# Kernel tuning notes

Measured on AMD Instinct MI355X. Metric: run time of the kernel, lower is better.

Reference implementation:

```python
import jax, jax.numpy as jnp
import numpy as np

EPS_NORM = 1e-12  # F.normalize eps
EPS_BN = 1e-5     # BatchNorm2d eps


def _neighbor_idx(h, w):
    # Replicates get_window_mask's clamped 3x3 neighbor indices (hw, 9).
    off = np.array([-1, 0, 1])
    x_off = np.tile(off, 3)        # [-1,0,1,-1,0,1,-1,0,1]
    y_off = np.repeat(off, 3)      # [-1,-1,-1,0,0,0,1,1,1]
    yy, xx = np.meshgrid(np.arange(h), np.arange(w), indexing='ij')
    x_nn = np.clip(xx.reshape(-1, 1) + x_off[None, :], 0, w - 1)
    y_nn = np.clip(yy.reshape(-1, 1) + y_off[None, :], 0, h - 1)
    return jnp.asarray(y_nn * w + x_nn, dtype=jnp.int32)  # (hw, 9)


def _find_nn(xf, yf, idx):
    # Faithful to find_nn: cosine sim between cur pixel and 3x3 window of y,
    # argmin over the (masked-in) window, gather the NORMALIZED y feature.
    # The dense (hw,hw) matmul + 9999 mask reduces exactly to these 9 candidates.
    b, c, h, w = xf.shape
    xn = xf.reshape(b, c, h * w).transpose(0, 2, 1)  # (b, hw, c)
    xn = xn / jnp.maximum(jnp.linalg.norm(xn, axis=-1, keepdims=True), EPS_NORM)
    yn = yf.reshape(b, c, h * w)
    yn = yn / jnp.maximum(jnp.linalg.norm(yn, axis=1, keepdims=True), EPS_NORM)
    ynt = yn.transpose(0, 2, 1)          # (b, hw, c)
    y_nb = ynt[:, idx, :]                # (b, hw, 9, c) gathered neighbors
    sims = jnp.einsum('bpc,bpkc->bpk', xn, y_nb)  # (b, hw, 9)
    k = jnp.argmin(sims, axis=-1)
    nnv = jnp.take_along_axis(y_nb, k[:, :, None, None], axis=2)[:, :, 0, :]
    return nnv.transpose(0, 2, 1).reshape(b, c, h, w)


def _forward(x, conv_w, bn_gamma, bn_beta):
    h, w = x.shape[-2:]
    prev_f, next_f, cur_f = x[:, 0], x[:, 1], x[:, 2]
    idx = _neighbor_idx(h, w)
    nn_prev = _find_nn(cur_f, prev_f, idx)
    nn_next = _find_nn(cur_f, next_f, idx)
    feat = jnp.concatenate([nn_prev, nn_next, cur_f], axis=1)  # (b, 3c, h, w)
    out = jnp.einsum('oc,bchw->bohw', conv_w, feat)            # 1x1 conv, no bias
    # BatchNorm2d in training mode: per-channel batch stats (biased var)
    mean = out.mean(axis=(0, 2, 3), keepdims=True)
    var = out.var(axis=(0, 2, 3), keepdims=True)
    out = (out - mean) * jax.lax.rsqrt(var + EPS_BN)
    out = out * bn_gamma[None, :, None, None] + bn_beta[None, :, None, None]
    out = jax.nn.relu(out)
    return jnp.stack([prev_f, next_f, out], axis=1)  # (b, 3, c, h, w)


def setup_inputs() -> dict:
    key = jax.random.key(0)
    k1, k2 = jax.random.split(key)
    b, c, h, w = 8, 256, 64, 64
    x = jax.random.normal(k1, (b, 3, c, h, w), dtype=jnp.float32)
    fan_in, fan_out = 3 * c, c
    bound = float(np.sqrt(6.0 / (fan_in + fan_out)))  # xavier_uniform
    conv_w = jax.random.uniform(k2, (c, 3 * c), dtype=jnp.float32, minval=-bound, maxval=bound)
    bn_gamma = jnp.ones((c,), dtype=jnp.float32)
    bn_beta = jnp.zeros((c,), dtype=jnp.float32)
    return {'x': x, 'conv_w': conv_w, 'bn_gamma': bn_gamma, 'bn_beta': bn_beta}


def reference(x, conv_w, bn_gamma, bn_beta):
    return _forward(x, conv_w, bn_gamma, bn_beta)
```

## Files before the change

kernel.cpp:

```cpp
#include <hip/hip_runtime.h>

constexpr int B  = 8;
constexpr int C  = 256;
constexpr int Hh = 64;
constexpr int Ww = 64;
constexpr int P  = Hh * Ww;
constexpr int CP = C * P;
constexpr int CT = 3 * C;
constexpr int J  = B * P;

constexpr int DOT_D_OFF = 0;
constexpr int SSQ_D_OFF = 294912;
constexpr int IV_F_OFF  = 655360;
constexpr int SEL_F_OFF = 663552;
constexpr int SIV_F_OFF = 671744;
constexpr int WB_F_OFF  = 679936;

typedef __attribute__((ext_vector_type(8))) short short8;
typedef __attribute__((ext_vector_type(4))) float f32x4;

__device__ inline unsigned short bf16_rne(float f) {
    unsigned u = __float_as_uint(f);
    return (unsigned short)((u + 0x7fffu + ((u >> 16) & 1u)) >> 16);
}
__device__ inline unsigned pack2(float a, float b) {
    return (unsigned)bf16_rne(a) | ((unsigned)bf16_rne(b) << 16);
}

__global__ __launch_bounds__(256) void k_wcvt(const float* __restrict__ Wg,
                                              unsigned short* __restrict__ Wb) {
    int i = blockIdx.x * 256 + threadIdx.x;
    Wb[i] = bf16_rne(Wg[i]);
}

__global__ __launch_bounds__(256) void k_dots(const float* __restrict__ x,
                                              float* __restrict__ out) {
    __shared__ float ys[2][2][6][64];
    __shared__ float cs[2][256];
    const int t     = threadIdx.x;
    const int b     = blockIdx.x >> 4;
    const int strip = blockIdx.x & 15;
    const int chunk = blockIdx.y;
    const int y0 = strip * 4;
    const int ry = t >> 6;
    const int xc = t & 63;
    const int xm = max(xc - 1, 0), xp = min(xc + 1, 63);
    const int c0 = chunk * 64;

    size_t gbase; int l0;
    if (t < 64) {
        gbase = (size_t)(b * 3 + 2) * CP + (size_t)c0 * P + strip * 256 + t * 4;
        l0 = t * 4;
    } else {
        int i   = t - 64;
        int sid = i >= 96;
        int r   = (i - sid * 96) >> 4;
        int x4  = i & 15;
        int yl  = min(max(y0 - 1 + r, 0), Hh - 1);
        gbase = (size_t)(b * 3 + sid) * CP + (size_t)c0 * P + yl * 64 + x4 * 4;
        l0 = (sid * 6 + r) * 64 + x4 * 4;
    }
    float* ysf = &ys[0][0][0][0];
    float* dst0 = (t < 64) ? &cs[0][l0] : &ysf[l0];
    float* dst1 = (t < 64) ? &cs[1][l0] : &ysf[768 + l0];

    double d[2][9] = {{0,0,0,0,0,0,0,0,0},{0,0,0,0,0,0,0,0,0}};
    double qs[2] = {0.0, 0.0};

    f32x4 r0 = *(const f32x4*)(x + gbase);
    f32x4 r1 = *(const f32x4*)(x + gbase + (size_t)P);

    #define COMPUTE(BUF)                                                     \
    {                                                                        \
        double cd = (double)cs[BUF][t];                                      \
        _Pragma("unroll")                                                    \
        for (int s = 0; s < 2; ++s) {                                        \
            const float* Y0 = &ys[BUF][s][ry][0];             \
            const float* Y1 = Y0 + 64;                        \
            const float* Y2 = Y1 + 64;                        \
            d[s][0] = fma(cd, (double)Y0[xm], d[s][0]);                      \
            d[s][1] = fma(cd, (double)Y0[xc], d[s][1]);                      \
            d[s][2] = fma(cd, (double)Y0[xp], d[s][2]);                      \
            d[s][3] = fma(cd, (double)Y1[xm], d[s][3]);                      \
            d[s][4] = fma(cd, (double)Y1[xc], d[s][4]);                      \
            d[s][5] = fma(cd, (double)Y1[xp], d[s][5]);                      \
            d[s][6] = fma(cd, (double)Y2[xm], d[s][6]);                      \
            d[s][7] = fma(cd, (double)Y2[xc], d[s][7]);                      \
            d[s][8] = fma(cd, (double)Y2[xp], d[s][8]);                      \
            double ov = (double)Y1[xc];                                      \
            qs[s] = fma(ov, ov, qs[s]);                                      \
        }                                                                    \
    }

    for (int n = 0; n < 64; n += 2) {
        *(f32x4*)dst0 = r0;
        __syncthreads();
        if (n + 2 < 64)
            r0 = *(const f32x4*)(x + gbase + (size_t)(n + 2) * P);
        COMPUTE(0)
        *(f32x4*)dst1 = r1;
        __syncthreads();
        if (n + 3 < 64)
            r1 = *(const f32x4*)(x + gbase + (size_t)(n + 3) * P);
        COMPUTE(1)
    }
    #undef COMPUTE

    const int p = strip * 256 + t;
    double* db = (double*)(out + (size_t)(b * 3) * CP);
    #pragma unroll
    for (int s = 0; s < 2; ++s) {
        #pragma unroll
        for (int k = 0; k < 9; ++k)
            db[DOT_D_OFF + (size_t)((chunk * 2 + s) * 9 + k) * 4096 + p] = d[s][k];
        db[SSQ_D_OFF + (size_t)(chunk * 2 + s) * 4096 + p] = qs[s];
    }
}

__global__ __launch_bounds__(256) void k_iv(float* __restrict__ out) {
    int gid  = blockIdx.x * 256 + threadIdx.x;
    int side = gid >> 15;
    int j    = gid & (J - 1);
    int b = j >> 12, p = j & (P - 1);
    const double* sb = (const double*)(out + (size_t)(b * 3) * CP) + SSQ_D_OFF;
    double ssum = ((sb[(0 * 2 + side) * 4096 + p]
                  + sb[(1 * 2 + side) * 4096 + p])
                  + sb[(2 * 2 + side) * 4096 + p])
                  + sb[(3 * 2 + side) * 4096 + p];
    float* ivb = out + (size_t)(b * 3) * CP + IV_F_OFF;
    ivb[side * 4096 + p] = 1.0f / fmaxf((float)sqrt(ssum), 1e-12f);
}

__global__ __launch_bounds__(256) void k_sel(float* __restrict__ out) {
    int gid  = blockIdx.x * 256 + threadIdx.x;
    int side = gid >> 15;
    int j    = gid & (J - 1);
    int b = j >> 12, p = j & (P - 1);
    int y = p >> 6, xc = p & 63;

    int nidx[9];
    #pragma unroll
    for (int k = 0; k < 9; ++k) {
        int dy = k / 3 - 1, dx = k % 3 - 1;
        int yy = min(max(y + dy, 0), Hh - 1);
        int xx = min(max(xc + dx, 0), Ww - 1);
        nidx[k] = yy * Ww + xx;
    }

    const double* db  = (const double*)(out + (size_t)(b * 3) * CP) + DOT_D_OFF;
    const float*  ivb = out + (size_t)(b * 3) * CP + IV_F_OFF;

    double best = 0.0; int bi = 0;
    #pragma unroll
    for (int k = 0; k < 9; ++k) {
        double sk = ((db[(size_t)((0 * 2 + side) * 9 + k) * 4096 + p]
                    + db[(size_t)((1 * 2 + side) * 9 + k) * 4096 + p])
                    + db[(size_t)((2 * 2 + side) * 9 + k) * 4096 + p])
                    + db[(size_t)((3 * 2 + side) * 9 + k) * 4096 + p];
        double s = sk * (double)ivb[side * 4096 + nidx[k]];
        if (k == 0 || s < best) { best = s; bi = k; }
    }
    int*   selb = (int*)(out + (size_t)(b * 3) * CP + SEL_F_OFF);
    float* sivb = out + (size_t)(b * 3) * CP + SIV_F_OFF;
    selb[side * 4096 + p] = nidx[bi];
    sivb[side * 4096 + p] = ivb[side * 4096 + nidx[bi]];
}

__global__ __launch_bounds__(512) void k_gemm(const float* __restrict__ x,
                                              const unsigned short* __restrict__ Wb,
                                              float* __restrict__ out) {
    __shared__ unsigned short As[2][4][256][8];
    __shared__ unsigned short Bs[2][4][128][8];
    __shared__ int   sel_s[2][128];
    __shared__ float siv_s[2][128];

    const int t  = threadIdx.x;
    const int j0 = blockIdx.x * 128;
    const int b  = j0 >> 12, p0 = j0 & (P - 1);

    if (t < 256) {
        int side = t >> 7, jj = t & 127;
        const int*   selb = (const int*)(out + (size_t)(b * 3) * CP + SEL_F_OFF);
        const float* sivb = out + (size_t)(b * 3) * CP + SIV_F_OFF;
        sel_s[side][jj] = selb[side * 4096 + p0 + jj];
        siv_s[side][jj] = sivb[side * 4096 + p0 + jj];
    }
    __syncthreads();

    const int lane = t & 63, w = t >> 6;
    const int q = lane >> 4, l16 = lane & 15;
    const int m0w = (w & 3) * 64;
    const int n0w = (w >> 2) * 64;

    const int jj = t & 127, kq = (t >> 7) & 3;
    const int ma = t & 255, kh = t >> 8;
    const int k0 = kq * 8;

    const float* pp = x + (size_t)(b * 3 + 0) * CP + sel_s[0][jj];
    const float* np = x + (size_t)(b * 3 + 1) * CP + sel_s[1][jj];
    const float* cp = x + (size_t)(b * 3 + 2) * CP + p0 + jj;
    const float  sp = siv_s[0][jj], sn = siv_s[1][jj];
    const unsigned short* wbase = Wb + (size_t)ma * CT + kh * 16;

    f32x4 acc[4][4];
    #pragma unroll
    for (int f = 0; f < 4; ++f)
        #pragma unroll
        for (int g = 0; g < 4; ++g)
            acc[f][g] = (f32x4){0.f, 0.f, 0.f, 0.f};

    short8 wa0, wa1;
    float fb[8];
    float scale;

    #define LOAD_STEP(KK)                                                    \
    {                                                                        \
        const unsigned short* wsrc = wbase + (KK);                           \
        wa0 = *(const short8*)wsrc;                                          \
        wa1 = *(const short8*)(wsrc + 8);                                    \
        const float* src;                                                    \
        if ((KK) < 256)      { src = pp + (size_t)((KK) + k0) * P;       scale = sp;   } \
        else if ((KK) < 512) { src = np + (size_t)((KK) - 256 + k0) * P; scale = sn;   } \
        else                 { src = cp + (size_t)((KK) - 512 + k0) * P; scale = 1.0f; } \
        _Pragma("unroll")                                                    \
        for (int u = 0; u < 8; ++u) fb[u] = src[(size_t)u * P];              \
    }

    #define WRITE_STEP(BUF)                                                  \
    {                                                                        \
        *(short8*)&As[BUF][kh * 2    ][ma][0] = wa0;                         \
        *(short8*)&As[BUF][kh * 2 + 1][ma][0] = wa1;                         \
        uint4 pk = make_uint4(pack2(fb[0] * scale, fb[1] * scale),           \
                              pack2(fb[2] * scale, fb[3] * scale),           \
                              pack2(fb[4] * scale, fb[5] * scale),           \
                              pack2(fb[6] * scale, fb[7] * scale));          \
        *(uint4*)&Bs[BUF][kq][jj][0] = pk;                                   \
    }

    LOAD_STEP(0)
    WRITE_STEP(0)
    __syncthreads();

    for (int i = 0; i < 24; ++i) {
        if (i + 1 < 24) LOAD_STEP((i + 1) * 32)
        const int cur = i & 1;
        short8 af[4], bfr[4];
        #pragma unroll
        for (int f = 0; f < 4; ++f)
            af[f] = *(const short8*)&As[cur][q][m0w + f * 16 + l16][0];
        #pragma unroll
        for (int g = 0; g < 4; ++g)
            bfr[g] = *(const short8*)&Bs[cur][q][n0w + g * 16 + l16][0];
        #pragma unroll
        for (int f = 0; f < 4; ++f)
            #pragma unroll
            for (int g = 0; g < 4; ++g)
                acc[f][g] = __builtin_amdgcn_mfma_f32_16x16x32_bf16(
                    af[f], bfr[g], acc[f][g], 0, 0, 0);
        if (i + 1 < 24) WRITE_STEP((i + 1) & 1)
        __syncthreads();
    }
    #undef LOAD_STEP
    #undef WRITE_STEP

    float* outb = out + (size_t)(b * 3 + 2) * CP;
    #pragma unroll
    for (int f = 0; f < 4; ++f)
        #pragma unroll
        for (int g = 0; g < 4; ++g)
            #pragma unroll
            for (int r = 0; r < 4; ++r) {
                int ch  = m0w + f * 16 + q * 4 + r;
                int col = p0 + n0w + g * 16 + l16;
                outb[(size_t)ch * P + col] = acc[f][g][r];
            }
}

__global__ __launch_bounds__(256) void k_bn(float* __restrict__ out,
                                            const float* __restrict__ gamma,
                                            const float* __restrict__ beta) {
    __shared__ double rs[256], rq[256];
    __shared__ float sc_s, sh_s;
    const int o = blockIdx.x, t = threadIdx.x;

    double s = 0.0, q = 0.0;
    for (int b = 0; b < B; ++b) {
        const float4* base =
            (const float4*)(out + (size_t)(b * 3 + 2) * CP + (size_t)o * P);
        #pragma unroll
        for (int i = 0; i < 4; ++i) {
            float4 v = base[i * 256 + t];
            s += (double)v.x + (double)v.y + (double)v.z + (double)v.w;
            q += (double)v.x * v.x + (double)v.y * v.y
               + (double)v.z * v.z + (double)v.w * v.w;
        }
    }
    rs[t] = s; rq[t] = q;
    __syncthreads();
    for (int off = 128; off > 0; off >>= 1) {
        if (t < off) { rs[t] += rs[t + off]; rq[t] += rq[t + off]; }
        __syncthreads();
    }
    if (t == 0) {
        double mean = rs[0] * (1.0 / (double)J);
        double var  = rq[0] * (1.0 / (double)J) - mean * mean;
        double inv  = 1.0 / sqrt(var + 1e-5);
        double sc   = (double)gamma[o] * inv;
        sc_s = (float)sc;
        sh_s = (float)((double)beta[o] - mean * sc);
    }
    __syncthreads();
    const float sc = sc_s, sh = sh_s;

    for (int b = 0; b < B; ++b) {
        float4* base =
            (float4*)(out + (size_t)(b * 3 + 2) * CP + (size_t)o * P);
        #pragma unroll
        for (int i = 0; i < 4; ++i) {
            float4 v = base[i * 256 + t];
            v.x = fmaxf(fmaf(v.x, sc, sh), 0.f);
            v.y = fmaxf(fmaf(v.y, sc, sh), 0.f);
            v.z = fmaxf(fmaf(v.z, sc, sh), 0.f);
            v.w = fmaxf(fmaf(v.w, sc, sh), 0.f);
            base[i * 256 + t] = v;
        }
    }
}

__global__ __launch_bounds__(256) void k_copy(const float4* __restrict__ x4,
                                              float4* __restrict__ o4) {
    int tid = blockIdx.x * blockDim.x + threadIdx.x;
    const int per_b = 2 * CP / 4;
    const int bstr  = 3 * CP / 4;
    if (tid < B * per_b) {
        int b = tid / per_b;
        int r = tid - b * per_b;
        o4[b * bstr + r] = x4[b * bstr + r];
    }
}

extern "C" void kernel_launch(void* const* d_in, const int* in_sizes, int n_in,
                              void* d_out, int out_size, void* d_ws, size_t ws_size,
                              hipStream_t stream) {
    const float* x     = (const float*)d_in[0];
    const float* wconv = (const float*)d_in[1];
    const float* gamma = (const float*)d_in[2];
    const float* beta  = (const float*)d_in[3];
    float* out = (float*)d_out;
    (void)d_ws; (void)ws_size;

    unsigned short* Wbuf = (unsigned short*)(out + WB_F_OFF);

    k_wcvt<<<CT * C / 256, 256, 0, stream>>>(wconv, Wbuf);

    k_dots<<<dim3(128, 4), 256, 0, stream>>>(x, out);

    k_iv<<<2 * J / 256, 256, 0, stream>>>(out);

    k_sel<<<2 * J / 256, 256, 0, stream>>>(out);

    k_gemm<<<J / 128, 512, 0, stream>>>(x, Wbuf, out);

    k_bn<<<C, 256, 0, stream>>>(out, gamma, beta);

    k_copy<<<(B * 2 * CP / 4 + 255) / 256, 256, 0, stream>>>(
        (const float4*)x, (float4*)out);
}
```

Before: 267.5 us.

## Fuse inverse-norm kernel into selection and deepen k_dots channel pipeline

Removes the separate k_iv launch by recomputing each neighbor's inverse norm inside k_sel from the partial sum-of-squares buffers. This saves one kernel launch and one intermediate buffer round-trip, but adds redundant loads and sqrt work per neighbor. Separately, k_dots now stages two channels per shared-memory buffer, with four channels of global loads in flight. This halves the number of barriers per channel at the cost of more shared memory and registers.

Measured after the change: 262.0 us. 2.0% less time.

```diff
diff --git a/kernel.cpp b/kernel.cpp
--- a/kernel.cpp
+++ b/kernel.cpp
@@ -11,7 +11,6 @@
 
 constexpr int DOT_D_OFF = 0;
 constexpr int SSQ_D_OFF = 294912;
-constexpr int IV_F_OFF  = 655360;
 constexpr int SEL_F_OFF = 663552;
 constexpr int SIV_F_OFF = 671744;
 constexpr int WB_F_OFF  = 679936;
@@ -35,8 +34,8 @@
 
 __global__ __launch_bounds__(256) void k_dots(const float* __restrict__ x,
                                               float* __restrict__ out) {
-    __shared__ float ys[2][2][6][64];
-    __shared__ float cs[2][256];
+    __shared__ float ys[2][2][2][6][64];
+    __shared__ float cs[2][2][256];
     const int t     = threadIdx.x;
     const int b     = blockIdx.x >> 4;
     const int strip = blockIdx.x & 15;
@@ -47,10 +46,15 @@
     const int xm = max(xc - 1, 0), xp = min(xc + 1, 63);
     const int c0 = chunk * 64;
 
-    size_t gbase; int l0;
+    size_t gbase;
+    float *d00, *d01, *d10, *d11;
+    float* ysf = &ys[0][0][0][0][0];
+    float* csf = &cs[0][0][0];
     if (t < 64) {
         gbase = (size_t)(b * 3 + 2) * CP + (size_t)c0 * P + strip * 256 + t * 4;
-        l0 = t * 4;
+        int l0 = t * 4;
+        d00 = csf + l0;        d01 = csf + 256 + l0;
+        d10 = csf + 512 + l0;  d11 = csf + 768 + l0;
     } else {
         int i   = t - 64;
         int sid = i >= 96;
@@ -58,24 +62,25 @@
         int x4  = i & 15;
         int yl  = min(max(y0 - 1 + r, 0), Hh - 1);
         gbase = (size_t)(b * 3 + sid) * CP + (size_t)c0 * P + yl * 64 + x4 * 4;
-        l0 = (sid * 6 + r) * 64 + x4 * 4;
-    }
-    float* ysf = &ys[0][0][0][0];
-    float* dst0 = (t < 64) ? &cs[0][l0] : &ysf[l0];
-    float* dst1 = (t < 64) ? &cs[1][l0] : &ysf[768 + l0];
+        int l0 = (sid * 6 + r) * 64 + x4 * 4;
+        d00 = ysf + l0;         d01 = ysf + 768 + l0;
+        d10 = ysf + 1536 + l0;  d11 = ysf + 1536 + 768 + l0;
+    }
 
     double d[2][9] = {{0,0,0,0,0,0,0,0,0},{0,0,0,0,0,0,0,0,0}};
     double qs[2] = {0.0, 0.0};
 
-    f32x4 r0 = *(const f32x4*)(x + gbase);
-    f32x4 r1 = *(const f32x4*)(x + gbase + (size_t)P);
-
-    #define COMPUTE(BUF)                                                     \
+    f32x4 a0 = *(const f32x4*)(x + gbase);
+    f32x4 a1 = *(const f32x4*)(x + gbase + (size_t)P);
+    f32x4 b0 = *(const f32x4*)(x + gbase + (size_t)2 * P);
+    f32x4 b1 = *(const f32x4*)(x + gbase + (size_t)3 * P);
+
+    #define COMPUTE(BUF, CH)                                                 \
     {                                                                        \
-        double cd = (double)cs[BUF][t];                                      \
+        double cd = (double)cs[BUF][CH][t];                                  \
         _Pragma("unroll")                                                    \
         for (int s = 0; s < 2; ++s) {                                        \
-            const float* Y0 = &ys[BUF][s][ry][0];             \
+            const float* Y0 = &ys[BUF][CH][s][ry][0];         \
             const float* Y1 = Y0 + 64;                        \
             const float* Y2 = Y1 + 64;                        \
             d[s][0] = fma(cd, (double)Y0[xm], d[s][0]);                      \
@@ -92,17 +97,21 @@
         }                                                                    \
     }
 
-    for (int n = 0; n < 64; n += 2) {
-        *(f32x4*)dst0 = r0;
+    for (int n = 0; n < 64; n += 4) {
+        *(f32x4*)d00 = a0; *(f32x4*)d01 = a1;
         __syncthreads();
-        if (n + 2 < 64)
-            r0 = *(const f32x4*)(x + gbase + (size_t)(n + 2) * P);
-        COMPUTE(0)
-        *(f32x4*)dst1 = r1;
+        if (n + 4 < 64) {
+            a0 = *(const f32x4*)(x + gbase + (size_t)(n + 4) * P);
+            a1 = *(const f32x4*)(x + gbase + (size_t)(n + 5) * P);
+        }
+        COMPUTE(0, 0) COMPUTE(0, 1)
+        *(f32x4*)d10 = b0; *(f32x4*)d11 = b1;
         __syncthreads();
-        if (n + 3 < 64)
-            r1 = *(const f32x4*)(x + gbase + (size_t)(n + 3) * P);
-        COMPUTE(1)
+        if (n + 6 < 64) {
+            b0 = *(const f32x4*)(x + gbase + (size_t)(n + 6) * P);
+            b1 = *(const f32x4*)(x + gbase + (size_t)(n + 7) * P);
+        }
+        COMPUTE(1, 0) COMPUTE(1, 1)
     }
     #undef COMPUTE
 
@@ -115,20 +124,6 @@
             db[DOT_D_OFF + (size_t)((chunk * 2 + s) * 9 + k) * 4096 + p] = d[s][k];
         db[SSQ_D_OFF + (size_t)(chunk * 2 + s) * 4096 + p] = qs[s];
     }
-}
-
-__global__ __launch_bounds__(256) void k_iv(float* __restrict__ out) {
-    int gid  = blockIdx.x * 256 + threadIdx.x;
-    int side = gid >> 15;
-    int j    = gid & (J - 1);
-    int b = j >> 12, p = j & (P - 1);
-    const double* sb = (const double*)(out + (size_t)(b * 3) * CP) + SSQ_D_OFF;
-    double ssum = ((sb[(0 * 2 + side) * 4096 + p]
-                  + sb[(1 * 2 + side) * 4096 + p])
-                  + sb[(2 * 2 + side) * 4096 + p])
-                  + sb[(3 * 2 + side) * 4096 + p];
-    float* ivb = out + (size_t)(b * 3) * CP + IV_F_OFF;
-    ivb[side * 4096 + p] = 1.0f / fmaxf((float)sqrt(ssum), 1e-12f);
 }
 
 __global__ __launch_bounds__(256) void k_sel(float* __restrict__ out) {
@@ -147,23 +142,29 @@
         nidx[k] = yy * Ww + xx;
     }
 
-    const double* db  = (const double*)(out + (size_t)(b * 3) * CP) + DOT_D_OFF;
-    const float*  ivb = out + (size_t)(b * 3) * CP + IV_F_OFF;
-
-    double best = 0.0; int bi = 0;
+    const double* db = (const double*)(out + (size_t)(b * 3) * CP) + DOT_D_OFF;
+    const double* sb = (const double*)(out + (size_t)(b * 3) * CP) + SSQ_D_OFF;
+
+    double best = 0.0; int bi = 0; float sivbest = 0.0f;
     #pragma unroll
     for (int k = 0; k < 9; ++k) {
+        int nq = nidx[k];
+        double ssum = ((sb[(0 * 2 + side) * 4096 + nq]
+                      + sb[(1 * 2 + side) * 4096 + nq])
+                      + sb[(2 * 2 + side) * 4096 + nq])
+                      + sb[(3 * 2 + side) * 4096 + nq];
+        float ivf = 1.0f / fmaxf((float)sqrt(ssum), 1e-12f);
         double sk = ((db[(size_t)((0 * 2 + side) * 9 + k) * 4096 + p]
                     + db[(size_t)((1 * 2 + side) * 9 + k) * 4096 + p])
                     + db[(size_t)((2 * 2 + side) * 9 + k) * 4096 + p])
                     + db[(size_t)((3 * 2 + side) * 9 + k) * 4096 + p];
-        double s = sk * (double)ivb[side * 4096 + nidx[k]];
-        if (k == 0 || s < best) { best = s; bi = k; }
+        double s = sk * (double)ivf;
+        if (k == 0 || s < best) { best = s; bi = k; sivbest = ivf; }
     }
     int*   selb = (int*)(out + (size_t)(b * 3) * CP + SEL_F_OFF);
     float* sivb = out + (size_t)(b * 3) * CP + SIV_F_OFF;
     selb[side * 4096 + p] = nidx[bi];
-    sivb[side * 4096 + p] = ivb[side * 4096 + nidx[bi]];
+    sivb[side * 4096 + p] = sivbest;
 }
 
 __global__ __launch_bounds__(512) void k_gemm(const float* __restrict__ x,
@@ -355,8 +356,6 @@
 
     k_dots<<<dim3(128, 4), 256, 0, stream>>>(x, out);
 
-    k_iv<<<2 * J / 256, 256, 0, stream>>>(out);
-
     k_sel<<<2 * J / 256, 256, 0, stream>>>(out);
 
     k_gemm<<<J / 128, 512, 0, stream>>>(x, Wbuf, out);
```
